# Kernel tuning notes

Hardware: AMD Instinct MI355X
Metric: run time of the kernel (lower is better)

Reference implementation:

```python
import jax, jax.numpy as jnp
import numpy as np

N, E = 16384, 262144
D_NODE, D_EDGE, H = 256, 64, 8
EPS = 1e-5

def _lin(key, din, dout):
    kw, kb = jax.random.split(key)
    s = 1.0 / np.sqrt(din)
    W = jax.random.uniform(kw, (din, dout), jnp.float32, -s, s)
    b = jax.random.uniform(kb, (dout,), jnp.float32, -s, s)
    return W, b

def setup_inputs() -> dict:
    key = jax.random.key(0)
    ks = jax.random.split(key, 12)
    node_features = jax.random.normal(ks[0], (N, D_NODE), jnp.float32)
    edge_index = jax.random.randint(ks[1], (2, E), 0, N, jnp.int64)
    edge_features = jax.random.normal(ks[2], (E, D_EDGE), jnp.float32)
    Wn, bn = _lin(ks[3], D_NODE, D_NODE)
    Wq, bq = _lin(ks[4], D_NODE, D_NODE)
    Wk, bk = _lin(ks[5], D_NODE, D_NODE)
    Wv, bv = _lin(ks[6], D_NODE, D_NODE)
    We, be = _lin(ks[7], D_EDGE, D_NODE)
    A1, a1 = _lin(ks[8], 3 * D_NODE, D_NODE)
    A2, a2 = _lin(ks[9], D_NODE, H)
    gamma = jnp.ones((D_NODE,), jnp.float32)
    beta = jnp.zeros((D_NODE,), jnp.float32)
    return dict(node_features=node_features, edge_index=edge_index,
                edge_features=edge_features, Wn=Wn, bn=bn, Wq=Wq, bq=bq,
                Wk=Wk, bk=bk, Wv=Wv, bv=bv, We=We, be=be,
                A1=A1, a1=a1, A2=A2, a2=a2, gamma=gamma, beta=beta)

def _leaky(x):
    return jnp.where(x > 0, x, 0.2 * x)

def reference(node_features, edge_index, edge_features, Wn, bn, Wq, bq,
              Wk, bk, Wv, bv, We, be, A1, a1, A2, a2, gamma, beta):
    h = node_features @ Wn + bn                      # [N, d]
    q = node_features @ Wq + bq
    k = node_features @ Wk + bk
    v = node_features @ Wv + bv
    edge_h = edge_features @ We + be                 # [E, d]
    src, tgt = edge_index[0], edge_index[1]
    attn_in = jnp.concatenate([q[src], k[tgt], edge_h], axis=-1)  # [E, 3d]
    scores = _leaky(_leaky(attn_in @ A1 + a1) @ A2 + a2)          # [E, H]
    # softmax over ALL edges (dim=0) of head-mean, as in the original
    w = jax.nn.softmax(scores.mean(axis=-1), axis=0)              # [E]
    out = jnp.zeros_like(node_features).at[src].add(w[:, None] * v[tgt])
    x = h + out                                      # dropout is identity (eval)
    mu = x.mean(-1, keepdims=True)
    var = ((x - mu) ** 2).mean(-1, keepdims=True)
    return (x - mu) / jnp.sqrt(var + EPS) * gamma + beta
```

## Files before the change

### kernel.cpp

```cpp
#include <hip/hip_runtime.h>
#include <stdint.h>

#define NN 16384
#define EE 262144
#define DD 256

typedef float f32x4 __attribute__((ext_vector_type(4)));
typedef float f32x2 __attribute__((ext_vector_type(2)));
typedef short s16x8 __attribute__((ext_vector_type(8)));
typedef unsigned short u16x4 __attribute__((ext_vector_type(4)));
typedef unsigned short u16x8 __attribute__((ext_vector_type(8)));

#define AS1 __attribute__((address_space(1)))
#define AS3 __attribute__((address_space(3)))

__device__ __forceinline__ float bf2f(unsigned short u) {
  union { unsigned int i; float f; } v; v.i = ((unsigned int)u) << 16; return v.f;
}
__device__ __forceinline__ unsigned short f2bf(float f) {
  union { float f; unsigned int i; } v; v.f = f;
  unsigned int r = v.i + 0x7fffu + ((v.i >> 16) & 1u);
  return (unsigned short)(r >> 16);
}
__device__ __forceinline__ float lrelu(float x) { return x > 0.f ? x : 0.2f * x; }

__device__ __forceinline__ uint8_t f2e4m3(float x) {
  uint32_t xu = __float_as_uint(x);
  uint32_t s = (xu >> 24) & 0x80u;
  float a = fabsf(x);
  if (a >= 448.f) return (uint8_t)(s | 0x7Eu);
  if (a < 0.015625f) return (uint8_t)s;
  uint32_t u = xu & 0x7FFFFFFFu;
  u = u + 0x0007FFFFu + ((u >> 20) & 1u);
  uint32_t E = (u >> 23) - 120u;
  if (E >= 16u) return (uint8_t)(s | 0x7Eu);
  return (uint8_t)(s | (E << 3) | ((u >> 20) & 7u));
}
__device__ __forceinline__ float e4m3f(uint32_t b) {
  uint32_t ex = b & 0x78u;
  uint32_t bits = ((b & 0x80u) << 24) | (((b & 0x7fu) << 20) + (120u << 23));
  union { uint32_t u; float f; } v;
  v.u = ex ? bits : ((b & 0x80u) << 24);
  return v.f;
}
#if defined(__has_builtin)
#if __has_builtin(__builtin_amdgcn_cvt_pk_f32_fp8)
#define HAVE_CVT_FP8 1
#endif
#endif
__device__ __forceinline__ void dec4(uint32_t w, float* f) {
#ifdef HAVE_CVT_FP8
  f32x2 lo = __builtin_amdgcn_cvt_pk_f32_fp8(w, false);
  f32x2 hi = __builtin_amdgcn_cvt_pk_f32_fp8(w, true);
  f[0] = lo[0]; f[1] = lo[1]; f[2] = hi[0]; f[3] = hi[1];
#else
  f[0] = e4m3f(w & 0xFFu); f[1] = e4m3f((w >> 8) & 0xFFu);
  f[2] = e4m3f((w >> 16) & 0xFFu); f[3] = e4m3f(w >> 24);
#endif
}
__device__ __forceinline__ void dec16(uint4 v, float* f) {
  dec4(v.x, f); dec4(v.y, f + 4); dec4(v.z, f + 8); dec4(v.w, f + 12);
}

__device__ __forceinline__ int chanperm(int c) {
  int hi = c & ~63, loc = c & 63;
  int ct = loc >> 4, quad = (loc >> 2) & 3, rr = loc & 3;
  return hi | (quad * 16 + ct * 4 + rr);
}

__global__ __launch_bounds__(256) void prep_hist_kernel(
    const float* __restrict__ Wn, const float* __restrict__ bn,
    const float* __restrict__ Wq, const float* __restrict__ bq,
    const float* __restrict__ Wk, const float* __restrict__ bk,
    const float* __restrict__ Wv, const float* __restrict__ bv,
    const float* __restrict__ We, const float* __restrict__ be,
    const float* __restrict__ A1, const float* __restrict__ a1,
    const float* __restrict__ A2, const int* __restrict__ eidx,
    unsigned short* __restrict__ BcatT, float* __restrict__ bcat,
    unsigned short* __restrict__ WeaT, float* __restrict__ bcomb,
    float* __restrict__ A2p, int* __restrict__ deg)
{
  const int b = blockIdx.x, t = threadIdx.x;
  if (b < 256) {
    float acc = 0.f;
    for (int j = 0; j < 256; ++j) acc += Wq[b * 256 + j] * A1[j * 256 + t];
    BcatT[(512 + t) * 256 + b] = f2bf(acc);
  } else if (b < 512) {
    int k = b - 256; float acc = 0.f;
    for (int j = 0; j < 256; ++j) acc += Wk[k * 256 + j] * A1[(256 + j) * 256 + t];
    BcatT[(768 + t) * 256 + k] = f2bf(acc);
  } else if (b < 576) {
    int k = b - 512; float acc = 0.f;
    for (int j = 0; j < 256; ++j) acc += We[k * 256 + j] * A1[(512 + j) * 256 + t];
    WeaT[chanperm(t) * 64 + k] = f2bf(acc);
  } else if (b == 576) {
    float acc = a1[t];
    for (int j = 0; j < 256; ++j) {
      acc += bq[j] * A1[j * 256 + t];
      acc += bk[j] * A1[(256 + j) * 256 + t];
      acc += be[j] * A1[(512 + j) * 256 + t];
    }
    bcomb[chanperm(t)] = acc;
  } else if (b < 705) {
    int b2 = b - 577;
    for (int rr = 0; rr < 4; ++rr) {
      int np = b2 * 4 + rr;
      float v = (np < 256) ? Wn[t * 256 + np] : Wv[t * 256 + (np - 256)];
      BcatT[np * 256 + t] = f2bf(v);
    }
  } else if (b == 705) {
    bcat[t] = bn[t];
    bcat[256 + t] = bv[t];
    bcat[512 + t] = 0.f;
    bcat[768 + t] = 0.f;
  } else if (b == 706) {
    int m = chanperm(t);
    for (int j = 0; j < 8; ++j) A2p[m * 8 + j] = A2[t * 8 + j];
  } else {
    int e = (b - 707) * 256 + t;
    atomicAdd(&deg[eidx[e]], 1);
  }
}

__global__ __launch_bounds__(256) void conv_scan_kernel(
    const float* __restrict__ in, unsigned short* __restrict__ o,
    const int* __restrict__ deg, int* __restrict__ startA,
    int* __restrict__ cursor)
{
  const int t = threadIdx.x;
  if (blockIdx.x < 2048) {
    size_t i = (size_t)blockIdx.x * 256 + t;
    const f32x4* p = (const f32x4*)(in + i * 8);
    f32x4 a = p[0], b = p[1];
    u16x8 r = { f2bf(a[0]), f2bf(a[1]), f2bf(a[2]), f2bf(a[3]),
                f2bf(b[0]), f2bf(b[1]), f2bf(b[2]), f2bf(b[3]) };
    *(u16x8*)(o + i * 8) = r;
    return;
  }
  __shared__ int ls[256];
  int4 d[16];
  int s = 0;
  #pragma unroll
  for (int i = 0; i < 16; ++i) {
    d[i] = ((const int4*)deg)[t * 16 + i];
    s += d[i].x + d[i].y + d[i].z + d[i].w;
  }
  ls[t] = s;
  __syncthreads();
  for (int dd = 1; dd < 256; dd <<= 1) {
    int v = ls[t];
    if (t >= dd) v += ls[t - dd];
    __syncthreads();
    ls[t] = v;
    __syncthreads();
  }
  int run = ls[t] - s;
  #pragma unroll
  for (int i = 0; i < 16; ++i) {
    int4 ov;
    ov.x = run; run += d[i].x;
    ov.y = run; run += d[i].y;
    ov.z = run; run += d[i].z;
    ov.w = run; run += d[i].w;
    ((int4*)startA)[t * 16 + i] = ov;
    ((int4*)cursor)[t * 16 + i] = ov;
  }
  if (t == 255) startA[NN] = run;
}

__global__ __launch_bounds__(256, 1) void gemm_perm_kernel(
    const unsigned short* __restrict__ Abf,
    const unsigned short* __restrict__ BT,
    const float* __restrict__ bias,
    unsigned short* __restrict__ hout, uint8_t* __restrict__ vq,
    uint8_t* __restrict__ Qaq, uint8_t* __restrict__ Kaq,
    const int* __restrict__ eidx, int* __restrict__ cursor,
    int* __restrict__ perm, int* __restrict__ srcp, int* __restrict__ tgtp)
{
  const int t = threadIdx.x;
  if (blockIdx.x < 1024) {
    int e = blockIdx.x * 256 + t;
    int s = eidx[e], tg = eidx[EE + e];
    int pos = atomicAdd(&cursor[s], 1);
    perm[pos] = e;
    srcp[pos] = s;
    tgtp[pos] = tg;
    return;
  }
  __shared__ __align__(16) unsigned short Al[128 * 64];
  __shared__ __align__(16) unsigned short Bl[128 * 64];
  const int b2 = blockIdx.x - 1024;
  const int wid = t >> 6, lane = t & 63;
  const int quad = lane >> 4, l15 = lane & 15;
  const int mblk = b2 & 127, nblk = b2 >> 7;
  const int m0 = mblk * 128, n0 = nblk * 128;
  const int mh = wid >> 1, nh = wid & 1;
  const int srow = lane >> 3, sslot = lane & 7;

  f32x4 acc[4][4];
  #pragma unroll
  for (int i = 0; i < 4; ++i)
    #pragma unroll
    for (int j = 0; j < 4; ++j) acc[i][j] = (f32x4){0.f, 0.f, 0.f, 0.f};

  for (int ks = 0; ks < 4; ++ks) {
    const int k0 = ks * 64;
    #pragma unroll
    for (int j = 0; j < 4; ++j) {
      int cj = wid * 4 + j;
      int row = cj * 8 + srow;
      const unsigned short* ga =
          Abf + (size_t)(m0 + row) * 256 + k0 + ((sslot ^ (row & 7)) * 8);
      __builtin_amdgcn_global_load_lds((AS1 const void*)ga,
                                       (AS3 void*)(Al + cj * 512), 16, 0, 0);
      const unsigned short* gb =
          BT + (size_t)(n0 + row) * 256 + k0 + ((sslot ^ (row & 7)) * 8);
      __builtin_amdgcn_global_load_lds((AS1 const void*)gb,
                                       (AS3 void*)(Bl + cj * 512), 16, 0, 0);
    }
    __syncthreads();
    s16x8 af[4][2], bfr[4][2];
    #pragma unroll
    for (int mt = 0; mt < 4; ++mt) {
      int row = mh * 64 + mt * 16 + l15;
      #pragma unroll
      for (int kk = 0; kk < 2; ++kk) {
        int s = (kk * 4 + quad) ^ (row & 7);
        af[mt][kk] = *(const s16x8*)(Al + row * 64 + s * 8);
      }
    }
    #pragma unroll
    for (int nt = 0; nt < 4; ++nt) {
      int row = nh * 64 + nt * 16 + l15;
      #pragma unroll
      for (int kk = 0; kk < 2; ++kk) {
        int s = (kk * 4 + quad) ^ (row & 7);
        bfr[nt][kk] = *(const s16x8*)(Bl + row * 64 + s * 8);
      }
    }
    #pragma unroll
    for (int mt = 0; mt < 4; ++mt)
      #pragma unroll
      for (int nt = 0; nt < 4; ++nt) {
        acc[mt][nt] = __builtin_amdgcn_mfma_f32_16x16x32_bf16(
            af[mt][0], bfr[nt][0], acc[mt][nt], 0, 0, 0);
        acc[mt][nt] = __builtin_amdgcn_mfma_f32_16x16x32_bf16(
            af[mt][1], bfr[nt][1], acc[mt][nt], 0, 0, 0);
      }
    __syncthreads();
  }

  #pragma unroll
  for (int nt = 0; nt < 4; ++nt) {
    int n = n0 + nh * 64 + nt * 16 + l15;
    float bb = bias[n];
    int seg = n >> 8;
    int ncol = n & 255;
    #pragma unroll
    for (int mt = 0; mt < 4; ++mt) {
      int m = m0 + mh * 64 + mt * 16 + quad * 4;
      f32x4 a = acc[mt][nt];
      #pragma unroll
      for (int r = 0; r < 4; ++r) {
        float val = a[r] + bb;
        size_t idx = (size_t)(m + r) * 256 + ncol;
        if (seg == 0) hout[idx] = f2bf(val);
        else if (seg == 1) vq[idx] = f2e4m3(val);
        else if (seg == 2) Qaq[idx] = f2e4m3(val);
        else Kaq[idx] = f2e4m3(val);
      }
    }
  }
}

__global__ __launch_bounds__(256, 4) void edge_scores_kernel(
    const int* __restrict__ perm, const int* __restrict__ srcp,
    const int* __restrict__ tgtp, const float* __restrict__ ef,
    const uint8_t* __restrict__ Qaq, const uint8_t* __restrict__ Kaq,
    const unsigned short* __restrict__ WeaT, const float* __restrict__ bcomb,
    const float* __restrict__ A2p, const float* __restrict__ a2g,
    float* __restrict__ Pp, float* __restrict__ Zpart)
{
  __shared__ __align__(16) unsigned short efl[64 * 64];
  __shared__ __align__(16) float A2l[8][260];
  __shared__ __align__(16) float pl[4 * 64 * 8];
  __shared__ __align__(16) float bcl[256];
  __shared__ int srcl[64], tgtl[64];
  const int t = threadIdx.x;
  const int wid = t >> 6, lane = t & 63, quad = lane >> 4, l15 = lane & 15;
  const int wg = ((blockIdx.x & 7) << 9) | (blockIdx.x >> 3);
  const int eb = wg * 64;
  const int r = t >> 2, q4 = t & 3;

  {
    const f32x4 x0 = *(const f32x4*)(A2p + t * 8);
    const f32x4 x1 = *(const f32x4*)(A2p + t * 8 + 4);
    A2l[0][t] = x0[0]; A2l[1][t] = x0[1]; A2l[2][t] = x0[2]; A2l[3][t] = x0[3];
    A2l[4][t] = x1[0]; A2l[5][t] = x1[1]; A2l[6][t] = x1[2]; A2l[7][t] = x1[3];
  }
  if (t < 64) ((f32x4*)bcl)[t] = ((const f32x4*)bcomb)[t];
  else if (t < 128) srcl[t - 64] = srcp[eb + (t - 64)];
  else if (t < 192) tgtl[t - 128] = tgtp[eb + (t - 128)];
  {
    int pe = __builtin_nontemporal_load(&perm[eb + r]);
    const f32x4* sp = (const f32x4*)(ef + (size_t)pe * 64 + q4 * 16);
    f32x4 v0 = __builtin_nontemporal_load(sp);
    f32x4 v1 = __builtin_nontemporal_load(sp + 1);
    f32x4 v2 = __builtin_nontemporal_load(sp + 2);
    f32x4 v3 = __builtin_nontemporal_load(sp + 3);
    u16x8 w0 = { f2bf(v0[0]), f2bf(v0[1]), f2bf(v0[2]), f2bf(v0[3]),
                 f2bf(v1[0]), f2bf(v1[1]), f2bf(v1[2]), f2bf(v1[3]) };
    u16x8 w1 = { f2bf(v2[0]), f2bf(v2[1]), f2bf(v2[2]), f2bf(v2[3]),
                 f2bf(v3[0]), f2bf(v3[1]), f2bf(v3[2]), f2bf(v3[3]) };
    int s0_ = (2 * q4) ^ (r & 7), s1_ = (2 * q4 + 1) ^ (r & 7);
    *(u16x8*)&efl[r * 64 + s0_ * 8] = w0;
    *(u16x8*)&efl[r * 64 + s1_ * 8] = w1;
  }
  s16x8 af0[4], af1[4];
  #pragma unroll
  for (int ct = 0; ct < 4; ++ct) {
    int ch = wid * 64 + ct * 16 + l15;
    af0[ct] = *(const s16x8*)(WeaT + ch * 64 + quad * 8);
    af1[ct] = *(const s16x8*)(WeaT + ch * 64 + 32 + quad * 8);
  }
  __syncthreads();

  f32x4 acc[4][4];
  {
    const int cb = wid * 64 + quad * 16;
    uint4 qv[4], kv[4];
    #pragma unroll
    for (int x = 0; x < 4; ++x) {
      int e = x * 16 + l15;
      qv[x] = *(const uint4*)(Qaq + (size_t)srcl[e] * 256 + cb);
      kv[x] = *(const uint4*)(Kaq + (size_t)tgtl[e] * 256 + cb);
    }
    #pragma unroll
    for (int x = 0; x < 4; ++x) {
      float qf[16], kf[16];
      dec16(qv[x], qf); dec16(kv[x], kf);
      #pragma unroll
      for (int ct = 0; ct < 4; ++ct)
        #pragma unroll
        for (int rr = 0; rr < 4; ++rr)
          acc[ct][x][rr] = qf[ct * 4 + rr] + kf[ct * 4 + rr];
    }
  }

  #pragma unroll
  for (int et = 0; et < 4; ++et) {
    int e = et * 16 + l15;
    s16x8 b0 = *(const s16x8*)(efl + e * 64 + ((quad ^ (e & 7)) * 8));
    s16x8 b1 = *(const s16x8*)(efl + e * 64 + (((4 + quad) ^ (e & 7)) * 8));
    #pragma unroll
    for (int ct = 0; ct < 4; ++ct) {
      acc[ct][et] = __builtin_amdgcn_mfma_f32_16x16x32_bf16(af0[ct], b0, acc[ct][et], 0, 0, 0);
      acc[ct][et] = __builtin_amdgcn_mfma_f32_16x16x32_bf16(af1[ct], b1, acc[ct][et], 0, 0, 0);
    }
  }

  float part[4][8];
  #pragma unroll
  for (int i = 0; i < 4; ++i)
    #pragma unroll
    for (int j = 0; j < 8; ++j) part[i][j] = 0.f;
  #pragma unroll
  for (int ct = 0; ct < 4; ++ct) {
    int chb = wid * 64 + ct * 16 + quad * 4;
    f32x4 bc = *(const f32x4*)&bcl[chb];
    float mv[4][4];
    #pragma unroll
    for (int et = 0; et < 4; ++et)
      #pragma unroll
      for (int rr = 0; rr < 4; ++rr)
        mv[et][rr] = lrelu(acc[ct][et][rr] + bc[rr]);
    #pragma unroll
    for (int hh = 0; hh < 8; ++hh) {
      f32x4 w = *(const f32x4*)&A2l[hh][chb];
      #pragma unroll
      for (int et = 0; et < 4; ++et)
        part[et][hh] += mv[et][0] * w[0] + mv[et][1] * w[1] +
                        mv[et][2] * w[2] + mv[et][3] * w[3];
    }
  }
  #pragma unroll
  for (int et = 0; et < 4; ++et)
    #pragma unroll
    for (int hh = 0; hh < 8; ++hh) {
      part[et][hh] += __shfl_xor(part[et][hh], 16);
      part[et][hh] += __shfl_xor(part[et][hh], 32);
    }
  if (quad == 0) {
    #pragma unroll
    for (int et = 0; et < 4; ++et) {
      f32x4 p0 = { part[et][0], part[et][1], part[et][2], part[et][3] };
      f32x4 p1 = { part[et][4], part[et][5], part[et][6], part[et][7] };
      int e = et * 16 + l15;
      *(f32x4*)&pl[(wid * 64 + e) * 8] = p0;
      *(f32x4*)&pl[(wid * 64 + e) * 8 + 4] = p1;
    }
  }
  __syncthreads();
  if (t < 64) {
    f32x4 t0 = {0.f, 0.f, 0.f, 0.f}, t1 = {0.f, 0.f, 0.f, 0.f};
    #pragma unroll
    for (int w2 = 0; w2 < 4; ++w2) {
      t0 += *(const f32x4*)&pl[(w2 * 64 + t) * 8];
      t1 += *(const f32x4*)&pl[(w2 * 64 + t) * 8 + 4];
    }
    const f32x4 a20 = *(const f32x4*)a2g;
    const f32x4 a21 = *(const f32x4*)(a2g + 4);
    float sacc = 0.f;
    #pragma unroll
    for (int j = 0; j < 4; ++j) {
      sacc += lrelu(t0[j] + a20[j]);
      sacc += lrelu(t1[j] + a21[j]);
    }
    float p = __expf(sacc * 0.125f);
    Pp[eb + t] = p;
    #pragma unroll
    for (int d = 1; d < 64; d <<= 1) p += __shfl_xor(p, d);
    if (t == 0) atomicAdd(&Zpart[wg & 63], p);
  }
}

__global__ __launch_bounds__(256) void scatter_ln_kernel(
    const int* __restrict__ startA, const float* __restrict__ Pp,
    const float* __restrict__ Zpart, const int* __restrict__ tgtp,
    const uint8_t* __restrict__ vq, const unsigned short* __restrict__ hbuf,
    const float* __restrict__ gamma, const float* __restrict__ beta,
    float* __restrict__ out)
{
  const int wid = threadIdx.x >> 6, lane = threadIdx.x & 63;
  const int n = blockIdx.x * 4 + wid;
  float zv = Zpart[lane];
  #pragma unroll
  for (int d = 1; d < 64; d <<= 1) zv += __shfl_xor(zv, d);
  const float invZ = 1.f / zv;
  const int s0 = startA[n], s1 = startA[n + 1];
  float a0 = 0.f, a1_ = 0.f, a2_ = 0.f, a3_ = 0.f;
  int i = s0;
  for (; i + 3 < s1; i += 4) {
    float w0 = Pp[i], w1 = Pp[i + 1], w2 = Pp[i + 2], w3 = Pp[i + 3];
    int t0 = tgtp[i], t1 = tgtp[i + 1], t2 = tgtp[i + 2], t3 = tgtp[i + 3];
    uint32_t e0 = *(const uint32_t*)(vq + (size_t)t0 * 256 + lane * 4);
    uint32_t e1 = *(const uint32_t*)(vq + (size_t)t1 * 256 + lane * 4);
    uint32_t e2 = *(const uint32_t*)(vq + (size_t)t2 * 256 + lane * 4);
    uint32_t e3 = *(const uint32_t*)(vq + (size_t)t3 * 256 + lane * 4);
    float f0[4], f1[4], f2[4], f3[4];
    dec4(e0, f0); dec4(e1, f1); dec4(e2, f2); dec4(e3, f3);
    a0 += w0 * f0[0] + w1 * f1[0] + w2 * f2[0] + w3 * f3[0];
    a1_ += w0 * f0[1] + w1 * f1[1] + w2 * f2[1] + w3 * f3[1];
    a2_ += w0 * f0[2] + w1 * f1[2] + w2 * f2[2] + w3 * f3[2];
    a3_ += w0 * f0[3] + w1 * f1[3] + w2 * f2[3] + w3 * f3[3];
  }
  for (; i < s1; ++i) {
    float w0 = Pp[i];
    uint32_t e0 = *(const uint32_t*)(vq + (size_t)tgtp[i] * 256 + lane * 4);
    float f0[4];
    dec4(e0, f0);
    a0 += w0 * f0[0]; a1_ += w0 * f0[1]; a2_ += w0 * f0[2]; a3_ += w0 * f0[3];
  }
  a0 *= invZ; a1_ *= invZ; a2_ *= invZ; a3_ *= invZ;
  u16x4 hv = __builtin_nontemporal_load(
      (const u16x4*)(hbuf + (size_t)n * 256 + lane * 4));
  float x0 = bf2f(hv[0]) + a0, x1 = bf2f(hv[1]) + a1_;
  float x2 = bf2f(hv[2]) + a2_, x3 = bf2f(hv[3]) + a3_;
  float sum = x0 + x1 + x2 + x3;
  float sq = x0 * x0 + x1 * x1 + x2 * x2 + x3 * x3;
  #pragma unroll
  for (int d = 1; d < 64; d <<= 1) { sum += __shfl_xor(sum, d); sq += __shfl_xor(sq, d); }
  float mu = sum * (1.f / 256.f);
  float var = sq * (1.f / 256.f) - mu * mu;
  float rstd = rsqrtf(var + 1e-5f);
  f32x4 g = *(const f32x4*)(gamma + lane * 4);
  f32x4 b = *(const f32x4*)(beta + lane * 4);
  f32x4 o;
  o[0] = (x0 - mu) * rstd * g[0] + b[0];
  o[1] = (x1 - mu) * rstd * g[1] + b[1];
  o[2] = (x2 - mu) * rstd * g[2] + b[2];
  o[3] = (x3 - mu) * rstd * g[3] + b[3];
  *(f32x4*)(out + (size_t)n * 256 + lane * 4) = o;
}

extern "C" void kernel_launch(void* const* d_in, const int* in_sizes, int n_in,
                              void* d_out, int out_size, void* d_ws, size_t ws_size,
                              hipStream_t stream)
{
  (void)in_sizes; (void)n_in; (void)out_size; (void)ws_size;
  const float* nf    = (const float*)d_in[0];
  const int*   eidx  = (const int*)  d_in[1];
  const float* ef    = (const float*)d_in[2];
  const float* Wn    = (const float*)d_in[3];
  const float* bn    = (const float*)d_in[4];
  const float* Wq    = (const float*)d_in[5];
  const float* bq    = (const float*)d_in[6];
  const float* Wk    = (const float*)d_in[7];
  const float* bk    = (const float*)d_in[8];
  const float* Wv    = (const float*)d_in[9];
  const float* bv    = (const float*)d_in[10];
  const float* We    = (const float*)d_in[11];
  const float* be    = (const float*)d_in[12];
  const float* A1    = (const float*)d_in[13];
  const float* a1    = (const float*)d_in[14];
  const float* A2    = (const float*)d_in[15];
  const float* a2    = (const float*)d_in[16];
  const float* gamma = (const float*)d_in[17];
  const float* beta  = (const float*)d_in[18];
  float* out = (float*)d_out;

  char* ws = (char*)d_ws;
  size_t off = 0;
  auto take = [&](size_t bytes) {
    size_t r = off; off += (bytes + 255) & ~(size_t)255; return r;
  };
  float* Zpart   = (float*)(ws + take(256));
  int*   deg     = (int*)  (ws + take((size_t)NN * 4));
  int*   startA  = (int*)  (ws + take((size_t)(NN + 1) * 4));
  int*   cursor  = (int*)  (ws + take((size_t)NN * 4));
  int*   perm    = (int*)  (ws + take((size_t)EE * 4));
  int*   srcp    = (int*)  (ws + take((size_t)EE * 4));
  int*   tgtp    = (int*)  (ws + take((size_t)EE * 4));
  float* Pp      = (float*)(ws + take((size_t)EE * 4));
  unsigned short* hbuf = (unsigned short*)(ws + take((size_t)NN * DD * 2));
  uint8_t* vqB   = (uint8_t*)(ws + take((size_t)NN * DD));
  uint8_t* QaB   = (uint8_t*)(ws + take((size_t)NN * DD));
  uint8_t* KaB   = (uint8_t*)(ws + take((size_t)NN * DD));
  unsigned short* BcatT = (unsigned short*)(ws + take((size_t)1024 * 256 * 2));
  float* bcat    = (float*)(ws + take(1024 * 4));
  unsigned short* WeaT  = (unsigned short*)(ws + take((size_t)256 * 64 * 2));
  float* bcomb   = (float*)(ws + take(256 * 4));
  float* A2p     = (float*)(ws + take(256 * 8 * 4));
  unsigned short* nfb   = (unsigned short*)(ws + take((size_t)NN * DD * 2));

  hipMemsetAsync(d_ws, 0, 256 + (size_t)NN * 4, stream);

  prep_hist_kernel<<<1731, 256, 0, stream>>>(Wn, bn, Wq, bq, Wk, bk, Wv, bv,
                                             We, be, A1, a1, A2, eidx,
                                             BcatT, bcat, WeaT, bcomb, A2p, deg);
  conv_scan_kernel<<<2049, 256, 0, stream>>>(nf, nfb, deg, startA, cursor);
  gemm_perm_kernel<<<2048, 256, 0, stream>>>(nfb, BcatT, bcat, hbuf, vqB,
                                             QaB, KaB, eidx, cursor,
                                             perm, srcp, tgtp);
  edge_scores_kernel<<<4096, 256, 0, stream>>>(perm, srcp, tgtp, ef, QaB, KaB,
                                               WeaT, bcomb, A2p, a2, Pp, Zpart);
  scatter_ln_kernel<<<NN / 4, 256, 0, stream>>>(startA, Pp, Zpart, tgtp,
                                                vqB, hbuf, gamma, beta, out);
}
```

Before: 343.8 us.

## Pack src/tgt indices, use per-block Z partials, and shrink edge-scores LDS

Source and target indices are stored interleaved as int2, so each is one 8-byte load instead of two separate streams. The edge-scores kernel now reduces per-wave head partials with LDS atomics into a smaller buffer and raises launch bounds to 8 blocks/SM. It writes one Z partial per block instead of doing global atomics, and each scatter block re-reduces all 4096 partials. The risks are LDS atomic contention, register pressure from the higher occupancy target, and redundant Z reduction in every scatter block.

```diff
diff --git a/kernel.cpp b/kernel.cpp
--- a/kernel.cpp
+++ b/kernel.cpp
@@ -175,7 +175,7 @@
     unsigned short* __restrict__ hout, uint8_t* __restrict__ vq,
     uint8_t* __restrict__ Qaq, uint8_t* __restrict__ Kaq,
     const int* __restrict__ eidx, int* __restrict__ cursor,
-    int* __restrict__ perm, int* __restrict__ srcp, int* __restrict__ tgtp)
+    int* __restrict__ perm, int2* __restrict__ st2)
 {
   const int t = threadIdx.x;
   if (blockIdx.x < 1024) {
@@ -183,8 +183,7 @@
     int s = eidx[e], tg = eidx[EE + e];
     int pos = atomicAdd(&cursor[s], 1);
     perm[pos] = e;
-    srcp[pos] = s;
-    tgtp[pos] = tg;
+    st2[pos] = make_int2(s, tg);
     return;
   }
   __shared__ __align__(16) unsigned short Al[128 * 64];
@@ -273,19 +272,19 @@
   }
 }
 
-__global__ __launch_bounds__(256, 4) void edge_scores_kernel(
-    const int* __restrict__ perm, const int* __restrict__ srcp,
-    const int* __restrict__ tgtp, const float* __restrict__ ef,
+__global__ __launch_bounds__(256, 8) void edge_scores_kernel(
+    const int* __restrict__ perm, const int2* __restrict__ st2,
+    const float* __restrict__ ef,
     const uint8_t* __restrict__ Qaq, const uint8_t* __restrict__ Kaq,
     const unsigned short* __restrict__ WeaT, const float* __restrict__ bcomb,
     const float* __restrict__ A2p, const float* __restrict__ a2g,
-    float* __restrict__ Pp, float* __restrict__ Zpart)
+    float* __restrict__ Pp, float* __restrict__ Zblk)
 {
   __shared__ __align__(16) unsigned short efl[64 * 64];
-  __shared__ __align__(16) float A2l[8][260];
-  __shared__ __align__(16) float pl[4 * 64 * 8];
+  __shared__ __align__(16) float A2l[8][256];
+  __shared__ __align__(16) float pl[64][8];
   __shared__ __align__(16) float bcl[256];
-  __shared__ int srcl[64], tgtl[64];
+  __shared__ __align__(8) int stl[2][64];
   const int t = threadIdx.x;
   const int wid = t >> 6, lane = t & 63, quad = lane >> 4, l15 = lane & 15;
   const int wg = ((blockIdx.x & 7) << 9) | (blockIdx.x >> 3);
@@ -298,9 +297,17 @@
     A2l[0][t] = x0[0]; A2l[1][t] = x0[1]; A2l[2][t] = x0[2]; A2l[3][t] = x0[3];
     A2l[4][t] = x1[0]; A2l[5][t] = x1[1]; A2l[6][t] = x1[2]; A2l[7][t] = x1[3];
   }
-  if (t < 64) ((f32x4*)bcl)[t] = ((const f32x4*)bcomb)[t];
-  else if (t < 128) srcl[t - 64] = srcp[eb + (t - 64)];
-  else if (t < 192) tgtl[t - 128] = tgtp[eb + (t - 128)];
+  if (t < 64) {
+    int64_t sv = __builtin_nontemporal_load(
+        (const int64_t*)st2 + (eb + t));
+    stl[0][t] = (int)(sv & 0xFFFFFFFFll);
+    stl[1][t] = (int)(sv >> 32);
+  } else if (t < 128) {
+    ((f32x4*)bcl)[t - 64] = ((const f32x4*)bcomb)[t - 64];
+  } else if (t < 192) {
+    ((f32x4*)pl)[(t - 128) * 2] = (f32x4){0.f, 0.f, 0.f, 0.f};
+    ((f32x4*)pl)[(t - 128) * 2 + 1] = (f32x4){0.f, 0.f, 0.f, 0.f};
+  }
   {
     int pe = __builtin_nontemporal_load(&perm[eb + r]);
     const f32x4* sp = (const f32x4*)(ef + (size_t)pe * 64 + q4 * 16);
@@ -332,8 +339,8 @@
     #pragma unroll
     for (int x = 0; x < 4; ++x) {
       int e = x * 16 + l15;
-      qv[x] = *(const uint4*)(Qaq + (size_t)srcl[e] * 256 + cb);
-      kv[x] = *(const uint4*)(Kaq + (size_t)tgtl[e] * 256 + cb);
+      qv[x] = *(const uint4*)(Qaq + (size_t)stl[0][e] * 256 + cb);
+      kv[x] = *(const uint4*)(Kaq + (size_t)stl[1][e] * 256 + cb);
     }
     #pragma unroll
     for (int x = 0; x < 4; ++x) {
@@ -393,21 +400,16 @@
   if (quad == 0) {
     #pragma unroll
     for (int et = 0; et < 4; ++et) {
-      f32x4 p0 = { part[et][0], part[et][1], part[et][2], part[et][3] };
-      f32x4 p1 = { part[et][4], part[et][5], part[et][6], part[et][7] };
       int e = et * 16 + l15;
-      *(f32x4*)&pl[(wid * 64 + e) * 8] = p0;
-      *(f32x4*)&pl[(wid * 64 + e) * 8 + 4] = p1;
+      #pragma unroll
+      for (int hh = 0; hh < 8; ++hh)
+        atomicAdd(&pl[e][hh], part[et][hh]);
     }
   }
   __syncthreads();
   if (t < 64) {
-    f32x4 t0 = {0.f, 0.f, 0.f, 0.f}, t1 = {0.f, 0.f, 0.f, 0.f};
-    #pragma unroll
-    for (int w2 = 0; w2 < 4; ++w2) {
-      t0 += *(const f32x4*)&pl[(w2 * 64 + t) * 8];
-      t1 += *(const f32x4*)&pl[(w2 * 64 + t) * 8 + 4];
-    }
+    f32x4 t0 = *(const f32x4*)&pl[t][0];
+    f32x4 t1 = *(const f32x4*)&pl[t][4];
     const f32x4 a20 = *(const f32x4*)a2g;
     const f32x4 a21 = *(const f32x4*)(a2g + 4);
     float sacc = 0.f;
@@ -417,32 +419,45 @@
       sacc += lrelu(t1[j] + a21[j]);
     }
     float p = __expf(sacc * 0.125f);
-    Pp[eb + t] = p;
+    __builtin_nontemporal_store(p, &Pp[eb + t]);
     #pragma unroll
     for (int d = 1; d < 64; d <<= 1) p += __shfl_xor(p, d);
-    if (t == 0) atomicAdd(&Zpart[wg & 63], p);
+    if (t == 0) Zblk[wg] = p;
   }
 }
 
 __global__ __launch_bounds__(256) void scatter_ln_kernel(
     const int* __restrict__ startA, const float* __restrict__ Pp,
-    const float* __restrict__ Zpart, const int* __restrict__ tgtp,
+    const float* __restrict__ Zblk, const int2* __restrict__ st2,
     const uint8_t* __restrict__ vq, const unsigned short* __restrict__ hbuf,
     const float* __restrict__ gamma, const float* __restrict__ beta,
     float* __restrict__ out)
 {
-  const int wid = threadIdx.x >> 6, lane = threadIdx.x & 63;
+  __shared__ float zsl[4];
+  const int t = threadIdx.x;
+  const int wid = t >> 6, lane = t & 63;
   const int n = blockIdx.x * 4 + wid;
-  float zv = Zpart[lane];
-  #pragma unroll
-  for (int d = 1; d < 64; d <<= 1) zv += __shfl_xor(zv, d);
-  const float invZ = 1.f / zv;
+  float zp = 0.f;
+  {
+    const f32x4* zb = (const f32x4*)Zblk;
+    #pragma unroll
+    for (int i = 0; i < 4; ++i) {
+      f32x4 v = zb[t * 4 + i];
+      zp += v[0] + v[1] + v[2] + v[3];
+    }
+  }
+  #pragma unroll
+  for (int d = 1; d < 64; d <<= 1) zp += __shfl_xor(zp, d);
+  if (lane == 0) zsl[wid] = zp;
+  __syncthreads();
+  const float invZ = 1.f / (zsl[0] + zsl[1] + zsl[2] + zsl[3]);
+
   const int s0 = startA[n], s1 = startA[n + 1];
   float a0 = 0.f, a1_ = 0.f, a2_ = 0.f, a3_ = 0.f;
   int i = s0;
   for (; i + 3 < s1; i += 4) {
     float w0 = Pp[i], w1 = Pp[i + 1], w2 = Pp[i + 2], w3 = Pp[i + 3];
-    int t0 = tgtp[i], t1 = tgtp[i + 1], t2 = tgtp[i + 2], t3 = tgtp[i + 3];
+    int t0 = st2[i].y, t1 = st2[i + 1].y, t2 = st2[i + 2].y, t3 = st2[i + 3].y;
     uint32_t e0 = *(const uint32_t*)(vq + (size_t)t0 * 256 + lane * 4);
     uint32_t e1 = *(const uint32_t*)(vq + (size_t)t1 * 256 + lane * 4);
     uint32_t e2 = *(const uint32_t*)(vq + (size_t)t2 * 256 + lane * 4);
@@ -456,7 +471,7 @@
   }
   for (; i < s1; ++i) {
     float w0 = Pp[i];
-    uint32_t e0 = *(const uint32_t*)(vq + (size_t)tgtp[i] * 256 + lane * 4);
+    uint32_t e0 = *(const uint32_t*)(vq + (size_t)st2[i].y * 256 + lane * 4);
     float f0[4];
     dec4(e0, f0);
     a0 += w0 * f0[0]; a1_ += w0 * f0[1]; a2_ += w0 * f0[2]; a3_ += w0 * f0[3];
@@ -514,14 +529,13 @@
   auto take = [&](size_t bytes) {
     size_t r = off; off += (bytes + 255) & ~(size_t)255; return r;
   };
-  float* Zpart   = (float*)(ws + take(256));
   int*   deg     = (int*)  (ws + take((size_t)NN * 4));
   int*   startA  = (int*)  (ws + take((size_t)(NN + 1) * 4));
   int*   cursor  = (int*)  (ws + take((size_t)NN * 4));
   int*   perm    = (int*)  (ws + take((size_t)EE * 4));
-  int*   srcp    = (int*)  (ws + take((size_t)EE * 4));
-  int*   tgtp    = (int*)  (ws + take((size_t)EE * 4));
+  int2*  st2     = (int2*) (ws + take((size_t)EE * 8));
   float* Pp      = (float*)(ws + take((size_t)EE * 4));
+  float* Zblk    = (float*)(ws + take(4096 * 4));
   unsigned short* hbuf = (unsigned short*)(ws + take((size_t)NN * DD * 2));
   uint8_t* vqB   = (uint8_t*)(ws + take((size_t)NN * DD));
   uint8_t* QaB   = (uint8_t*)(ws + take((size_t)NN * DD));
@@ -533,7 +547,7 @@
   float* A2p     = (float*)(ws + take(256 * 8 * 4));
   unsigned short* nfb   = (unsigned short*)(ws + take((size_t)NN * DD * 2));
 
-  hipMemsetAsync(d_ws, 0, 256 + (size_t)NN * 4, stream);
+  (void)hipMemsetAsync(d_ws, 0, (size_t)NN * 4, stream);
 
   prep_hist_kernel<<<1731, 256, 0, stream>>>(Wn, bn, Wq, bq, Wk, bk, Wv, bv,
                                              We, be, A1, a1, A2, eidx,
@@ -541,9 +555,9 @@
   conv_scan_kernel<<<2049, 256, 0, stream>>>(nf, nfb, deg, startA, cursor);
   gemm_perm_kernel<<<2048, 256, 0, stream>>>(nfb, BcatT, bcat, hbuf, vqB,
                                              QaB, KaB, eidx, cursor,
-                                             perm, srcp, tgtp);
-  edge_scores_kernel<<<4096, 256, 0, stream>>>(perm, srcp, tgtp, ef, QaB, KaB,
-                                               WeaT, bcomb, A2p, a2, Pp, Zpart);
-  scatter_ln_kernel<<<NN / 4, 256, 0, stream>>>(startA, Pp, Zpart, tgtp,
+                                             perm, st2);
+  edge_scores_kernel<<<4096, 256, 0, stream>>>(perm, st2, ef, QaB, KaB,
+                                               WeaT, bcomb, A2p, a2, Pp, Zblk);
+  scatter_ln_kernel<<<NN / 4, 256, 0, stream>>>(startA, Pp, Zblk, st2,
                                                 vqB, hbuf, gamma, beta, out);
 }
```

Result: slower. 505.1 us (+46.9%).
